# Kernel tuning notes

Hardware: AMD Instinct MI355X
Metric: run time of the kernel (lower is better)

## Reference

```python
import jax, jax.numpy as jnp
import numpy as np

VOCAB = 50257
EMB = 512


def setup_inputs() -> dict:
    key = jax.random.key(0)
    k1, k2, k3 = jax.random.split(key, 3)
    input_token_ids = jax.random.randint(k1, (8, 4096), 0, VOCAB, dtype=jnp.int64 if jax.config.jax_enable_x64 else jnp.int32)
    W = jax.random.normal(k2, (EMB, VOCAB), dtype=jnp.float32)  # nn.Linear(vocab, emb).weight
    b = jax.random.normal(k3, (EMB,), dtype=jnp.float32)        # nn.Linear bias
    return {"input_token_ids": input_token_ids, "W": W, "b": b}


def reference(input_token_ids, W, b):
    # one_hot(ids, V) @ W.T + b  ==  W.T[ids] + b   (exact same math, gather form)
    scale = jnp.asarray(EMB, W.dtype) ** 0.5
    emb = jnp.take(W.T, input_token_ids, axis=0)  # [B, S, EMB]
    return (emb + b) * scale
```

## Files before the change

kernel.cpp:

```cpp
#include <hip/hip_runtime.h>


constexpr int VOCAB = 50257;
constexpr int EMB   = 512;
constexpr int NTOK  = 8 * 4096;
constexpr float SCALE = 22.62741699796952f;

constexpr int VB   = 64;
constexpr int NB   = (VOCAB + VB - 1) / VB;
constexpr int CAP  = 96;
constexpr int ECH  = 256;


__global__ __launch_bounds__(256) void build_buckets(
    const int* __restrict__ ids,
    int* __restrict__ counts,
    int* __restrict__ olist,
    int* __restrict__ buckets)
{
    int t = blockIdx.x * 256 + threadIdx.x;
    int id = ids[t];
    int bkt = id >> 6;
    int slot = atomicAdd(&counts[bkt], 1);
    if (slot < CAP) {
        buckets[bkt * CAP + slot] = (t << 6) | (id & 63);
    } else {
        int o = atomicAdd(&counts[NB], 1);
        olist[o] = t;
    }
}

__global__ __launch_bounds__(512) void scatter_main(
    const float* __restrict__ W,
    const float* __restrict__ bias,
    const int*   __restrict__ counts,
    const int*   __restrict__ buckets,
    const int*   __restrict__ olist,
    const int*   __restrict__ ids,
    float*       __restrict__ out)
{
    __shared__ float tile[ECH * VB];

    const int bid  = blockIdx.x;
    const int b    = bid >> 1;
    const int z    = bid & 1;
    const int tid  = threadIdx.x;
    const int lane = tid & 63;
    const int w    = tid >> 6;

    const int e0     = z * ECH;
    const int vstart = min(b * VB, VOCAB - VB);
    const int vadj   = b * VB - vstart;

    const int cnt   = min(counts[b], CAP);
    const int tok_a = buckets[b * CAP + lane];
    const int tok_b = buckets[b * CAP + 64 + (lane & 31)];
    const float4 b4 = *reinterpret_cast<const float4*>(bias + e0 + 4 * lane);

    #pragma unroll
    for (int p = 0; p < 32; ++p) {
        const int r = w * 32 + p;
        const int srccol = (lane - (r >> 2)) & 63;
        const float* gp = W + (size_t)(e0 + r) * VOCAB + (vstart + srccol);
        float* lp = &tile[r * VB];
        __builtin_amdgcn_global_load_lds(
            (const __attribute__((address_space(1))) void*)gp,
            (__attribute__((address_space(3))) void*)lp, 4, 0, 0);
    }
    __syncthreads();

    for (int i = w; i < cnt; i += 8) {
        const int pk = (i < 64) ? __builtin_amdgcn_readlane(tok_a, i)
                                : __builtin_amdgcn_readlane(tok_b, i - 64);
        const int t  = pk >> 6;
        const int vl = (pk & 63) + vadj;
        const int s  = (vl + lane) & 63;
        float4 o;
        o.x = tile[(4 * lane + 0) * VB + s];
        o.y = tile[(4 * lane + 1) * VB + s];
        o.z = tile[(4 * lane + 2) * VB + s];
        o.w = tile[(4 * lane + 3) * VB + s];
        o.x = (o.x + b4.x) * SCALE;
        o.y = (o.y + b4.y) * SCALE;
        o.z = (o.z + b4.z) * SCALE;
        o.w = (o.w + b4.w) * SCALE;
        *reinterpret_cast<float4*>(out + (size_t)t * EMB + e0 + 4 * lane) = o;
    }

    if (b == 0) {
        int n = counts[NB];
        for (int ww = w; ww < n; ww += 8) {
            int t  = olist[ww];
            int id = ids[t];
            #pragma unroll
            for (int m = 0; m < 4; ++m) {
                int e = e0 + lane + m * 64;
                out[(size_t)t * EMB + e] = (W[(size_t)e * VOCAB + id] + bias[e]) * SCALE;
            }
        }
    }
}

__global__ __launch_bounds__(256) void embed_gather(
    const int*   __restrict__ ids,
    const float* __restrict__ W,
    const float* __restrict__ b,
    float*       __restrict__ out)
{
    int idx4 = blockIdx.x * blockDim.x + threadIdx.x;
    int t    = idx4 >> 7;
    int e    = (idx4 & 127) << 2;
    int id = ids[t];
    float4 bb = *reinterpret_cast<const float4*>(b + e);
    const float* wcol = W + (size_t)id;
    float4 o;
    o.x = (wcol[(size_t)(e + 0) * VOCAB] + bb.x) * SCALE;
    o.y = (wcol[(size_t)(e + 1) * VOCAB] + bb.y) * SCALE;
    o.z = (wcol[(size_t)(e + 2) * VOCAB] + bb.z) * SCALE;
    o.w = (wcol[(size_t)(e + 3) * VOCAB] + bb.w) * SCALE;
    *reinterpret_cast<float4*>(out + (size_t)idx4 * 4) = o;
}

extern "C" void kernel_launch(void* const* d_in, const int* in_sizes, int n_in,
                              void* d_out, int out_size, void* d_ws, size_t ws_size,
                              hipStream_t stream)
{
    const int*   ids  = (const int*)  d_in[0];
    const float* W    = (const float*)d_in[1];
    const float* bias = (const float*)d_in[2];
    float*       out  = (float*)d_out;

    const size_t ws_ints_needed = (size_t)NB + 1 + NTOK + (size_t)NB * CAP;

    if (ws_size >= ws_ints_needed * sizeof(int)) {
        int* counts  = (int*)d_ws;
        int* olist   = counts + NB + 1;
        int* buckets = olist + NTOK;

        hipMemsetAsync(counts, 0, (NB + 1) * sizeof(int), stream);
        build_buckets<<<NTOK / 256, 256, 0, stream>>>(ids, counts, olist, buckets);
        scatter_main<<<NB * 2, 512, 0, stream>>>(W, bias, counts, buckets,
                                                 olist, ids, out);
    } else {
        constexpr int total4 = NTOK * EMB / 4;
        embed_gather<<<total4 / 256, 256, 0, stream>>>(ids, W, bias, out);
    }
}
```

Measured before the change: 195.0 us.

## Widen vocab buckets to 256 and split embedding into 64-row chunks with padded LDS tile

Measured after the change: 203.6 us. 4.4% more time.

```diff
diff --git a/kernel.cpp b/kernel.cpp
--- a/kernel.cpp
+++ b/kernel.cpp
@@ -6,10 +6,12 @@
 constexpr int NTOK  = 8 * 4096;
 constexpr float SCALE = 22.62741699796952f;
 
-constexpr int VB   = 64;
+constexpr int VB   = 256;
 constexpr int NB   = (VOCAB + VB - 1) / VB;
-constexpr int CAP  = 96;
-constexpr int ECH  = 256;
+constexpr int CAP  = 256;
+constexpr int ECH  = 64;
+constexpr int RSD  = VB + 1;
+constexpr int SMEM_BYTES = (ECH * RSD + CAP) * 4;
 
 
 __global__ __launch_bounds__(256) void build_buckets(
@@ -20,10 +22,10 @@
 {
     int t = blockIdx.x * 256 + threadIdx.x;
     int id = ids[t];
-    int bkt = id >> 6;
+    int bkt = id >> 8;
     int slot = atomicAdd(&counts[bkt], 1);
     if (slot < CAP) {
-        buckets[bkt * CAP + slot] = (t << 6) | (id & 63);
+        buckets[bkt * CAP + slot] = (t << 8) | (id & 255);
     } else {
         int o = atomicAdd(&counts[NB], 1);
         olist[o] = t;
@@ -39,52 +41,47 @@
     const int*   __restrict__ ids,
     float*       __restrict__ out)
 {
-    __shared__ float tile[ECH * VB];
+    extern __shared__ float smem[];
+    float* tile = smem;
+    int*   toks = (int*)(smem + ECH * RSD);
 
     const int bid  = blockIdx.x;
-    const int b    = bid >> 1;
-    const int z    = bid & 1;
+    const int b    = bid >> 3;
+    const int ec   = bid & 7;
+    const int e0   = ec * ECH;
     const int tid  = threadIdx.x;
     const int lane = tid & 63;
     const int w    = tid >> 6;
 
-    const int e0     = z * ECH;
     const int vstart = min(b * VB, VOCAB - VB);
     const int vadj   = b * VB - vstart;
 
-    const int cnt   = min(counts[b], CAP);
-    const int tok_a = buckets[b * CAP + lane];
-    const int tok_b = buckets[b * CAP + 64 + (lane & 31)];
-    const float4 b4 = *reinterpret_cast<const float4*>(bias + e0 + 4 * lane);
+    const int cnt = min(counts[b], CAP);
+    if (tid < CAP) toks[tid] = buckets[b * CAP + tid];
+    const float be = bias[e0 + lane];
 
     #pragma unroll
-    for (int p = 0; p < 32; ++p) {
-        const int r = w * 32 + p;
-        const int srccol = (lane - (r >> 2)) & 63;
-        const float* gp = W + (size_t)(e0 + r) * VOCAB + (vstart + srccol);
-        float* lp = &tile[r * VB];
-        __builtin_amdgcn_global_load_lds(
-            (const __attribute__((address_space(1))) void*)gp,
-            (__attribute__((address_space(3))) void*)lp, 4, 0, 0);
+    for (int p = 0; p < 8; ++p) {
+        const int r = w * 8 + p;
+        const size_t rowbase = (size_t)(e0 + r) * VOCAB + vstart;
+        #pragma unroll
+        for (int q = 0; q < 4; ++q) {
+            const float* gp = W + rowbase + q * 64 + lane;
+            float* lp = &tile[r * RSD + q * 64];
+            __builtin_amdgcn_global_load_lds(
+                (const __attribute__((address_space(1))) void*)gp,
+                (__attribute__((address_space(3))) void*)lp, 4, 0, 0);
+        }
     }
     __syncthreads();
 
+    const float* tl   = &tile[lane * RSD];
+    float*       outp = out + e0 + lane;
     for (int i = w; i < cnt; i += 8) {
-        const int pk = (i < 64) ? __builtin_amdgcn_readlane(tok_a, i)
-                                : __builtin_amdgcn_readlane(tok_b, i - 64);
-        const int t  = pk >> 6;
-        const int vl = (pk & 63) + vadj;
-        const int s  = (vl + lane) & 63;
-        float4 o;
-        o.x = tile[(4 * lane + 0) * VB + s];
-        o.y = tile[(4 * lane + 1) * VB + s];
-        o.z = tile[(4 * lane + 2) * VB + s];
-        o.w = tile[(4 * lane + 3) * VB + s];
-        o.x = (o.x + b4.x) * SCALE;
-        o.y = (o.y + b4.y) * SCALE;
-        o.z = (o.z + b4.z) * SCALE;
-        o.w = (o.w + b4.w) * SCALE;
-        *reinterpret_cast<float4*>(out + (size_t)t * EMB + e0 + 4 * lane) = o;
+        const int pk = toks[i];
+        const int t  = pk >> 8;
+        const int vl = (pk & 255) + vadj;
+        outp[(size_t)t * EMB] = (tl[vl] + be) * SCALE;
     }
 
     if (b == 0) {
@@ -92,11 +89,8 @@
         for (int ww = w; ww < n; ww += 8) {
             int t  = olist[ww];
             int id = ids[t];
-            #pragma unroll
-            for (int m = 0; m < 4; ++m) {
-                int e = e0 + lane + m * 64;
-                out[(size_t)t * EMB + e] = (W[(size_t)e * VOCAB + id] + bias[e]) * SCALE;
-            }
+            int e  = e0 + lane;
+            out[(size_t)t * EMB + e] = (W[(size_t)e * VOCAB + id] + bias[e]) * SCALE;
         }
     }
 }
@@ -139,8 +133,8 @@
 
         hipMemsetAsync(counts, 0, (NB + 1) * sizeof(int), stream);
         build_buckets<<<NTOK / 256, 256, 0, stream>>>(ids, counts, olist, buckets);
-        scatter_main<<<NB * 2, 512, 0, stream>>>(W, bias, counts, buckets,
-                                                 olist, ids, out);
+        scatter_main<<<NB * 8, 512, SMEM_BYTES, stream>>>(W, bias, counts, buckets,
+                                                          olist, ids, out);
     } else {
         constexpr int total4 = NTOK * EMB / 4;
         embed_gather<<<total4 / 256, 256, 0, stream>>>(ids, W, bias, out);
```
